# Optimization experiments

Hardware: AMD Instinct MI355X
Metric: run time of the kernel (lower is better)

The kernel has to match this reference:

```python
import jax, jax.numpy as jnp
import numpy as np

NEG_INF = -1e30  # stand-in for float('-inf'); avoids inf-inf NaN edge cases, same softmax result


def setup_inputs() -> dict:
    key = jax.random.key(0)
    k1, k2, k3, k4, k5 = jax.random.split(key, 5)
    B, T, C, H = 16, 2048, 200, 64
    x = jax.random.normal(k1, (B, T, C), dtype=jnp.float32)
    # padding mask over key positions, broadcastable to [B, T, T]
    padding_mask = jax.random.randint(k2, (B, 1, T), 0, 2, dtype=jnp.int32)
    # nn.Linear(n_embd, head_size, bias=False) weights, stored as [C, H] so y = x @ W
    Wk = jax.random.normal(k3, (C, H), dtype=jnp.float32) * (C ** -0.5)
    Wq = jax.random.normal(k4, (C, H), dtype=jnp.float32) * (C ** -0.5)
    Wv = jax.random.normal(k5, (C, H), dtype=jnp.float32) * (C ** -0.5)
    return {"x": x, "padding_mask": padding_mask, "Wk": Wk, "Wq": Wq, "Wv": Wv}


def reference(x, padding_mask, Wk, Wq, Wv):
    # x: [B,T,C]; padding_mask: [B,1,T] (0 = padded key position)
    k = x @ Wk  # [B,T,H]
    q = x @ Wq  # [B,T,H]
    v = x @ Wv  # [B,T,H]
    scale = k.shape[-1] ** -0.5
    wei = jnp.einsum("bqh,bkh->bqk", q, k) * scale  # [B,T,T]
    # mask padded key columns before softmax
    wei = jnp.where(padding_mask == 0, NEG_INF, wei)
    wei = jax.nn.softmax(wei, axis=-1)
    # mask padded query rows (transpose of padding mask) to exact zero after softmax
    mask_t = jnp.swapaxes(padding_mask, -2, -1)  # [B,T,1]
    wei = jnp.where(mask_t == 0, 0.0, wei)
    # dropout is identity in eval mode
    out = jnp.einsum("bqk,bkh->bqh", wei, v)  # [B,T,H]
    return out
```

## Files before the change

### kernel.cpp

```cpp
#include <hip/hip_runtime.h>


typedef __attribute__((ext_vector_type(8))) __bf16 bf16x8;
typedef __attribute__((ext_vector_type(4))) __bf16 bf16x4;
typedef __attribute__((ext_vector_type(4))) float f32x4;

#define T_SEQ 2048
#define C_DIM 200
#define H_DIM 64
#define BT_TOT 32768
#define QKV_ELEMS 2097152
#define PPAD 72
#define OPAD 68
#define WTF_FULL 36864
#define WTF_ELEMS 38400
#define WTF_A_ELEMS 24576
#define LOG2E 1.44269504088896f

__global__ void prep_w(const float* __restrict__ Wk, const float* __restrict__ Wq,
                       const float* __restrict__ Wv, __bf16* __restrict__ WtF) {
    int idx = blockIdx.x * 256 + threadIdx.x;
    if (idx >= WTF_ELEMS) return;
    int w, c, h;
    if (idx < WTF_FULL) {
        int j = idx & 7, lane = (idx >> 3) & 63;
        int chunk = idx >> 9;
        int t = chunk & 3, rest = chunk >> 2;
        w = rest % 3; int ks = rest / 3;
        c = ks * 32 + (lane >> 4) * 8 + j;
        h = t * 16 + (lane & 15);
    } else {
        int i2 = idx - WTF_FULL;
        int j = i2 & 7, l15 = (i2 >> 3) & 15, t = (i2 >> 7) & 3;
        w = i2 >> 9;
        c = 192 + j;
        h = t * 16 + l15;
    }
    const float* W = (w == 0) ? Wq : (w == 1) ? Wk : Wv;
    float val = W[c * H_DIM + h];
    if (w == 0) val *= 0.125f * LOG2E;
    WtF[idx] = (__bf16)val;
}

__global__ __launch_bounds__(256) void qkv_proj(const float* __restrict__ x,
                                                const __bf16* __restrict__ WtF,
                                                __bf16* __restrict__ qb,
                                                __bf16* __restrict__ kb,
                                                __bf16* __restrict__ vT) {
    __shared__ __bf16 Wl[WTF_A_ELEMS];

    const int tid = threadIdx.x;
    const int wave = tid >> 6, lane = tid & 63, l15 = lane & 15, quad = lane >> 4;
    const int m0b = blockIdx.x * 64;
    const int row0 = m0b + wave * 16;

    f32x4 acc[3][4] = {};

    #pragma unroll
    for (int i = 0; i < 12; ++i) {
        const int c = i * 256 + tid;
        *(bf16x8*)(Wl + c * 8) = *(const bf16x8*)(WtF + c * 8);
    }
    __syncthreads();
    #pragma unroll
    for (int ks = 0; ks < 4; ++ks) {
        const float* xr = x + (size_t)(row0 + l15) * C_DIM + ks * 32 + quad * 8;
        const float4 f0 = *(const float4*)xr;
        const float4 f1 = *(const float4*)(xr + 4);
        bf16x8 a;
        a[0]=(__bf16)f0.x; a[1]=(__bf16)f0.y; a[2]=(__bf16)f0.z; a[3]=(__bf16)f0.w;
        a[4]=(__bf16)f1.x; a[5]=(__bf16)f1.y; a[6]=(__bf16)f1.z; a[7]=(__bf16)f1.w;
        #pragma unroll
        for (int w = 0; w < 3; ++w)
            #pragma unroll
            for (int t = 0; t < 4; ++t) {
                const bf16x8 bf = *(const bf16x8*)(Wl + ((ks * 12 + w * 4 + t) << 9) + lane * 8);
                acc[w][t] = __builtin_amdgcn_mfma_f32_16x16x32_bf16(a, bf, acc[w][t], 0, 0, 0);
            }
    }
    __syncthreads();

    #pragma unroll
    for (int i = 0; i < 7; ++i) {
        const int c = i * 256 + tid;
        if (c < 1728)
            *(bf16x8*)(Wl + c * 8) = *(const bf16x8*)(WtF + WTF_A_ELEMS + c * 8);
    }
    __syncthreads();
    #pragma unroll
    for (int ks = 4; ks < 7; ++ks) {
        bf16x8 a;
        if (ks < 6 || quad == 0) {
            const float* xr = x + (size_t)(row0 + l15) * C_DIM + ks * 32 + quad * 8;
            const float4 f0 = *(const float4*)xr;
            const float4 f1 = *(const float4*)(xr + 4);
            a[0]=(__bf16)f0.x; a[1]=(__bf16)f0.y; a[2]=(__bf16)f0.z; a[3]=(__bf16)f0.w;
            a[4]=(__bf16)f1.x; a[5]=(__bf16)f1.y; a[6]=(__bf16)f1.z; a[7]=(__bf16)f1.w;
        } else {
            #pragma unroll
            for (int j = 0; j < 8; ++j) a[j] = (__bf16)0.f;
        }
        #pragma unroll
        for (int w = 0; w < 3; ++w)
            #pragma unroll
            for (int t = 0; t < 4; ++t) {
                const int off = (ks < 6) ? (((ks - 4) * 12 + w * 4 + t) << 9) + lane * 8
                                         : 12288 + ((w * 4 + t) << 7) + l15 * 8;
                const bf16x8 bf = *(const bf16x8*)(Wl + off);
                acc[w][t] = __builtin_amdgcn_mfma_f32_16x16x32_bf16(a, bf, acc[w][t], 0, 0, 0);
            }
    }

    #pragma unroll
    for (int t = 0; t < 4; ++t)
        #pragma unroll
        for (int r = 0; r < 4; ++r) {
            const size_t m = row0 + quad * 4 + r;
            qb[m * H_DIM + t * 16 + l15] = (__bf16)acc[0][t][r];
            kb[m * H_DIM + t * 16 + l15] = (__bf16)acc[1][t][r];
        }
    __syncthreads();
    #pragma unroll
    for (int t = 0; t < 4; ++t)
        #pragma unroll
        for (int r = 0; r < 4; ++r)
            Wl[(t * 16 + l15) * 72 + wave * 16 + quad * 4 + r] = (__bf16)acc[2][t][r];
    __syncthreads();
    const int bb = m0b >> 11, tloc = m0b & 2047;
    #pragma unroll
    for (int i = 0; i < 2; ++i) {
        const int seg = i * 256 + tid;
        const int h = seg >> 3, s8 = seg & 7;
        *(bf16x8*)(vT + ((size_t)bb * H_DIM + h) * T_SEQ + tloc + s8 * 8) =
            *(const bf16x8*)(Wl + h * 72 + s8 * 8);
    }
}

__global__ __launch_bounds__(256, 2) void attn(const __bf16* __restrict__ qb,
                                               const __bf16* __restrict__ kb,
                                               const __bf16* __restrict__ vT,
                                               const int* __restrict__ pm,
                                               float* __restrict__ out) {
    __shared__ __align__(16) char arena[8192 + 36864];
    float* biasS = (float*)arena;

    const int tid = threadIdx.x;
    const int wave = tid >> 6, lane = tid & 63, l15 = lane & 15, quad = lane >> 4;
    const int ks = wave;
    const int b = blockIdx.y;
    const int q0 = blockIdx.x * 64;
    const size_t bT = (size_t)b * T_SEQ;

    for (int i = tid; i < 512; i += 256) {
        const int4 p4 = *(const int4*)(pm + bT + i * 4);
        biasS[i * 4 + 0] = p4.x ? 0.f : -1e30f;
        biasS[i * 4 + 1] = p4.y ? 0.f : -1e30f;
        biasS[i * 4 + 2] = p4.z ? 0.f : -1e30f;
        biasS[i * 4 + 3] = p4.w ? 0.f : -1e30f;
    }
    __syncthreads();

    bf16x8 qa[4][2];
    #pragma unroll
    for (int mt = 0; mt < 4; ++mt)
        #pragma unroll
        for (int s = 0; s < 2; ++s)
            qa[mt][s] = *(const bf16x8*)(qb + (bT + q0 + mt * 16 + l15) * H_DIM + s * 32 + quad * 8);

    __bf16* P = (__bf16*)(arena + 8192) + wave * (64 * PPAD);
    const __bf16* kbase = kb + bT * H_DIM;
    const __bf16* vbase = vT + (size_t)b * H_DIM * T_SEQ;

    f32x4 oacc[4][4] = {};
    float lsum[4] = {0.f, 0.f, 0.f, 0.f};

    bf16x8 kf[8];
    #pragma unroll
    for (int n = 0; n < 4; ++n)
        #pragma unroll
        for (int s = 0; s < 2; ++s)
            kf[n * 2 + s] = *(const bf16x8*)(kbase + (ks * 512 + n * 16 + l15) * H_DIM + s * 32 + quad * 8);

    for (int kt = 0; kt < 8; ++kt) {
        const int key0 = ks * 512 + kt * 64;

        bf16x8 vf[8];
        #pragma unroll
        for (int t = 0; t < 4; ++t)
            #pragma unroll
            for (int s = 0; s < 2; ++s)
                vf[t * 2 + s] = *(const bf16x8*)(vbase + (size_t)(t * 16 + l15) * T_SEQ + key0 + s * 32 + quad * 8);

        #pragma unroll
        for (int n = 0; n < 4; ++n) {
            const f32x4 bias = *(const f32x4*)(biasS + key0 + n * 16 + quad * 4);
            f32x4 s_[4];
            #pragma unroll
            for (int mt = 0; mt < 4; ++mt) s_[mt] = bias;
            #pragma unroll
            for (int s = 0; s < 2; ++s)
                #pragma unroll
                for (int mt = 0; mt < 4; ++mt)
                    s_[mt] = __builtin_amdgcn_mfma_f32_16x16x32_bf16(kf[n * 2 + s], qa[mt][s], s_[mt], 0, 0, 0);
            #pragma unroll
            for (int mt = 0; mt < 4; ++mt) {
                bf16x4 p4;
                #pragma unroll
                for (int r = 0; r < 4; ++r) {
                    const float e = exp2f(s_[mt][r]);
                    lsum[mt] += e;
                    p4[r] = (__bf16)e;
                }
                *(bf16x4*)(P + (mt * 16 + l15) * PPAD + n * 16 + quad * 4) = p4;
            }
        }

        const int keyn = ks * 512 + ((kt < 7) ? kt + 1 : 7) * 64;
        #pragma unroll
        for (int n = 0; n < 4; ++n)
            #pragma unroll
            for (int s = 0; s < 2; ++s)
                kf[n * 2 + s] = *(const bf16x8*)(kbase + (keyn + n * 16 + l15) * H_DIM + s * 32 + quad * 8);

        bf16x8 pa[4][2];
        #pragma unroll
        for (int mt = 0; mt < 4; ++mt)
            #pragma unroll
            for (int s = 0; s < 2; ++s)
                pa[mt][s] = *(const bf16x8*)(P + (mt * 16 + l15) * PPAD + s * 32 + quad * 8);

        #pragma unroll
        for (int t = 0; t < 4; ++t)
            #pragma unroll
            for (int s = 0; s < 2; ++s)
                #pragma unroll
                for (int mt = 0; mt < 4; ++mt)
                    oacc[mt][t] = __builtin_amdgcn_mfma_f32_16x16x32_bf16(pa[mt][s], vf[t * 2 + s], oacc[mt][t], 0, 0, 0);
    }

    #pragma unroll
    for (int mt = 0; mt < 4; ++mt) {
        lsum[mt] += __shfl_xor(lsum[mt], 16, 64);
        lsum[mt] += __shfl_xor(lsum[mt], 32, 64);
    }

    float* Ocomb = (float*)(arena + 8192);
    float* Lcomb = Ocomb + 64 * OPAD;

    __syncthreads();
    if (ks == 1) {
        #pragma unroll
        for (int mt = 0; mt < 4; ++mt) {
            #pragma unroll
            for (int t = 0; t < 4; ++t)
                #pragma unroll
                for (int r = 0; r < 4; ++r)
                    Ocomb[(mt * 16 + quad * 4 + r) * OPAD + t * 16 + l15] = oacc[mt][t][r];
            if (quad == 0) Lcomb[mt * 16 + l15] = lsum[mt];
        }
    }
    __syncthreads();
    if (ks == 2) {
        #pragma unroll
        for (int mt = 0; mt < 4; ++mt) {
            #pragma unroll
            for (int t = 0; t < 4; ++t)
                #pragma unroll
                for (int r = 0; r < 4; ++r)
                    Ocomb[(mt * 16 + quad * 4 + r) * OPAD + t * 16 + l15] += oacc[mt][t][r];
            if (quad == 0) Lcomb[mt * 16 + l15] += lsum[mt];
        }
    }
    __syncthreads();
    if (ks == 3) {
        #pragma unroll
        for (int mt = 0; mt < 4; ++mt) {
            #pragma unroll
            for (int t = 0; t < 4; ++t)
                #pragma unroll
                for (int r = 0; r < 4; ++r)
                    Ocomb[(mt * 16 + quad * 4 + r) * OPAD + t * 16 + l15] += oacc[mt][t][r];
            if (quad == 0) Lcomb[mt * 16 + l15] += lsum[mt];
        }
    }
    __syncthreads();
    if (ks == 0) {
        #pragma unroll
        for (int mt = 0; mt < 4; ++mt) {
            lsum[mt] += Lcomb[mt * 16 + l15];
            #pragma unroll
            for (int t = 0; t < 4; ++t)
                #pragma unroll
                for (int r = 0; r < 4; ++r)
                    oacc[mt][t][r] += Ocomb[(mt * 16 + quad * 4 + r) * OPAD + t * 16 + l15];
            #pragma unroll
            for (int r = 0; r < 4; ++r) {
                const int qpos = q0 + mt * 16 + quad * 4 + r;
                const float lv = __shfl(lsum[mt], quad * 4 + r, 64);
                const bool qvalid = biasS[qpos] == 0.f;
                const float inv = (qvalid && lv > 0.f) ? 1.f / lv : 0.f;
                #pragma unroll
                for (int t = 0; t < 4; ++t)
                    out[(bT + qpos) * H_DIM + t * 16 + l15] = oacc[mt][t][r] * inv;
            }
        }
    }
}

extern "C" void kernel_launch(void* const* d_in, const int* in_sizes, int n_in,
                              void* d_out, int out_size, void* d_ws, size_t ws_size,
                              hipStream_t stream) {
    const float* x  = (const float*)d_in[0];
    const int* pm   = (const int*)d_in[1];
    const float* Wk = (const float*)d_in[2];
    const float* Wq = (const float*)d_in[3];
    const float* Wv = (const float*)d_in[4];
    float* out = (float*)d_out;

    __bf16* qb  = (__bf16*)d_ws;
    __bf16* kb  = qb + QKV_ELEMS;
    __bf16* vT  = kb + QKV_ELEMS;
    __bf16* WtF = vT + QKV_ELEMS;

    prep_w<<<dim3((WTF_ELEMS + 255) / 256), dim3(256), 0, stream>>>(Wk, Wq, Wv, WtF);
    qkv_proj<<<dim3(BT_TOT / 64), dim3(256), 0, stream>>>(x, WtF, qb, kb, vT);
    attn<<<dim3(T_SEQ / 64, 16), dim3(256), 0, stream>>>(qb, kb, vT, pm, out);
}
```

Baseline: 124.5 us.

## Enlarge QKV projection blocks, stage outputs in LDS, compute row sums via MFMA

```diff
diff --git a/kernel.cpp b/kernel.cpp
--- a/kernel.cpp
+++ b/kernel.cpp
@@ -42,23 +42,24 @@
     WtF[idx] = (__bf16)val;
 }
 
-__global__ __launch_bounds__(256) void qkv_proj(const float* __restrict__ x,
-                                                const __bf16* __restrict__ WtF,
-                                                __bf16* __restrict__ qb,
-                                                __bf16* __restrict__ kb,
-                                                __bf16* __restrict__ vT) {
-    __shared__ __bf16 Wl[WTF_A_ELEMS];
+__global__ __launch_bounds__(512, 2) void qkv_proj(const float* __restrict__ x,
+                                                   const __bf16* __restrict__ WtF,
+                                                   __bf16* __restrict__ qb,
+                                                   __bf16* __restrict__ kb,
+                                                   __bf16* __restrict__ vT) {
+    __shared__ __align__(16) char qarena[55296];
+    __bf16* Wl = (__bf16*)qarena;
 
     const int tid = threadIdx.x;
     const int wave = tid >> 6, lane = tid & 63, l15 = lane & 15, quad = lane >> 4;
-    const int m0b = blockIdx.x * 64;
+    const int m0b = blockIdx.x * 128;
     const int row0 = m0b + wave * 16;
 
     f32x4 acc[3][4] = {};
 
     #pragma unroll
-    for (int i = 0; i < 12; ++i) {
-        const int c = i * 256 + tid;
+    for (int i = 0; i < 6; ++i) {
+        const int c = i * 512 + tid;
         *(bf16x8*)(Wl + c * 8) = *(const bf16x8*)(WtF + c * 8);
     }
     __syncthreads();
@@ -81,8 +82,8 @@
     __syncthreads();
 
     #pragma unroll
-    for (int i = 0; i < 7; ++i) {
-        const int c = i * 256 + tid;
+    for (int i = 0; i < 4; ++i) {
+        const int c = i * 512 + tid;
         if (c < 1728)
             *(bf16x8*)(Wl + c * 8) = *(const bf16x8*)(WtF + WTF_A_ELEMS + c * 8);
     }
@@ -111,32 +112,47 @@
             }
     }
 
-    #pragma unroll
-    for (int t = 0; t < 4; ++t)
-        #pragma unroll
-        for (int r = 0; r < 4; ++r) {
-            const size_t m = row0 + quad * 4 + r;
-            qb[m * H_DIM + t * 16 + l15] = (__bf16)acc[0][t][r];
-            kb[m * H_DIM + t * 16 + l15] = (__bf16)acc[1][t][r];
-        }
-    __syncthreads();
-    #pragma unroll
-    for (int t = 0; t < 4; ++t)
-        #pragma unroll
-        for (int r = 0; r < 4; ++r)
-            Wl[(t * 16 + l15) * 72 + wave * 16 + quad * 4 + r] = (__bf16)acc[2][t][r];
-    __syncthreads();
-    const int bb = m0b >> 11, tloc = m0b & 2047;
-    #pragma unroll
-    for (int i = 0; i < 2; ++i) {
-        const int seg = i * 256 + tid;
-        const int h = seg >> 3, s8 = seg & 7;
-        *(bf16x8*)(vT + ((size_t)bb * H_DIM + h) * T_SEQ + tloc + s8 * 8) =
-            *(const bf16x8*)(Wl + h * 72 + s8 * 8);
+    __syncthreads();
+    {
+        __bf16* Lq = (__bf16*)qarena;
+        __bf16* Lk = Lq + 9216;
+        __bf16* Lv = Lk + 9216;
+        #pragma unroll
+        for (int t = 0; t < 4; ++t)
+            #pragma unroll
+            for (int r = 0; r < 4; ++r) {
+                const int mloc = wave * 16 + quad * 4 + r;
+                Lq[mloc * 72 + t * 16 + l15] = (__bf16)acc[0][t][r];
+                Lk[mloc * 72 + t * 16 + l15] = (__bf16)acc[1][t][r];
+                Lv[(t * 16 + l15) * 136 + mloc] = (__bf16)acc[2][t][r];
+            }
+    }
+    __syncthreads();
+    {
+        const __bf16* Lq = (const __bf16*)qarena;
+        const __bf16* Lk = Lq + 9216;
+        const __bf16* Lv = Lk + 9216;
+        const int bb = m0b >> 11, tloc = m0b & 2047;
+        #pragma unroll
+        for (int i = 0; i < 2; ++i) {
+            const int seg = i * 512 + tid;
+            const int row = seg >> 3, s8 = seg & 7;
+            *(bf16x8*)(qb + (size_t)(m0b + row) * H_DIM + s8 * 8) =
+                *(const bf16x8*)(Lq + row * 72 + s8 * 8);
+            *(bf16x8*)(kb + (size_t)(m0b + row) * H_DIM + s8 * 8) =
+                *(const bf16x8*)(Lk + row * 72 + s8 * 8);
+        }
+        #pragma unroll
+        for (int i = 0; i < 2; ++i) {
+            const int seg = i * 512 + tid;
+            const int h = seg >> 4, s16 = seg & 15;
+            *(bf16x8*)(vT + ((size_t)bb * H_DIM + h) * T_SEQ + tloc + s16 * 8) =
+                *(const bf16x8*)(Lv + h * 136 + s16 * 8);
+        }
     }
 }
 
-__global__ __launch_bounds__(256, 2) void attn(const __bf16* __restrict__ qb,
+__global__ __launch_bounds__(256, 3) void attn(const __bf16* __restrict__ qb,
                                                const __bf16* __restrict__ kb,
                                                const __bf16* __restrict__ vT,
                                                const int* __restrict__ pm,
@@ -167,33 +183,27 @@
         for (int s = 0; s < 2; ++s)
             qa[mt][s] = *(const bf16x8*)(qb + (bT + q0 + mt * 16 + l15) * H_DIM + s * 32 + quad * 8);
 
+    bf16x8 ones;
+    #pragma unroll
+    for (int j = 0; j < 8; ++j) ones[j] = (__bf16)1.0f;
+
     __bf16* P = (__bf16*)(arena + 8192) + wave * (64 * PPAD);
     const __bf16* kbase = kb + bT * H_DIM;
     const __bf16* vbase = vT + (size_t)b * H_DIM * T_SEQ;
 
     f32x4 oacc[4][4] = {};
-    float lsum[4] = {0.f, 0.f, 0.f, 0.f};
-
-    bf16x8 kf[8];
-    #pragma unroll
-    for (int n = 0; n < 4; ++n)
-        #pragma unroll
-        for (int s = 0; s < 2; ++s)
-            kf[n * 2 + s] = *(const bf16x8*)(kbase + (ks * 512 + n * 16 + l15) * H_DIM + s * 32 + quad * 8);
+    f32x4 oaccL[4] = {};
 
     for (int kt = 0; kt < 8; ++kt) {
         const int key0 = ks * 512 + kt * 64;
 
-        bf16x8 vf[8];
-        #pragma unroll
-        for (int t = 0; t < 4; ++t)
-            #pragma unroll
-            for (int s = 0; s < 2; ++s)
-                vf[t * 2 + s] = *(const bf16x8*)(vbase + (size_t)(t * 16 + l15) * T_SEQ + key0 + s * 32 + quad * 8);
-
         #pragma unroll
         for (int n = 0; n < 4; ++n) {
             const f32x4 bias = *(const f32x4*)(biasS + key0 + n * 16 + quad * 4);
+            bf16x8 kf[2];
+            #pragma unroll
+            for (int s = 0; s < 2; ++s)
+                kf[s] = *(const bf16x8*)(kbase + (key0 + n * 16 + l15) * H_DIM + s * 32 + quad * 8);
             f32x4 s_[4];
             #pragma unroll
             for (int mt = 0; mt < 4; ++mt) s_[mt] = bias;
@@ -201,27 +211,17 @@
             for (int s = 0; s < 2; ++s)
                 #pragma unroll
                 for (int mt = 0; mt < 4; ++mt)
-                    s_[mt] = __builtin_amdgcn_mfma_f32_16x16x32_bf16(kf[n * 2 + s], qa[mt][s], s_[mt], 0, 0, 0);
+                    s_[mt] = __builtin_amdgcn_mfma_f32_16x16x32_bf16(kf[s], qa[mt][s], s_[mt], 0, 0, 0);
             #pragma unroll
             for (int mt = 0; mt < 4; ++mt) {
                 bf16x4 p4;
                 #pragma unroll
-                for (int r = 0; r < 4; ++r) {
-                    const float e = exp2f(s_[mt][r]);
-                    lsum[mt] += e;
-                    p4[r] = (__bf16)e;
-                }
+                for (int r = 0; r < 4; ++r)
+                    p4[r] = (__bf16)exp2f(s_[mt][r]);
                 *(bf16x4*)(P + (mt * 16 + l15) * PPAD + n * 16 + quad * 4) = p4;
             }
         }
 
-        const int keyn = ks * 512 + ((kt < 7) ? kt + 1 : 7) * 64;
-        #pragma unroll
-        for (int n = 0; n < 4; ++n)
-            #pragma unroll
-            for (int s = 0; s < 2; ++s)
-                kf[n * 2 + s] = *(const bf16x8*)(kbase + (keyn + n * 16 + l15) * H_DIM + s * 32 + quad * 8);
-
         bf16x8 pa[4][2];
         #pragma unroll
         for (int mt = 0; mt < 4; ++mt)
@@ -230,22 +230,27 @@
                 pa[mt][s] = *(const bf16x8*)(P + (mt * 16 + l15) * PPAD + s * 32 + quad * 8);
 
         #pragma unroll
-        for (int t = 0; t < 4; ++t)
+        for (int s = 0; s < 2; ++s)
+            #pragma unroll
+            for (int mt = 0; mt < 4; ++mt)
+                oaccL[mt] = __builtin_amdgcn_mfma_f32_16x16x32_bf16(pa[mt][s], ones, oaccL[mt], 0, 0, 0);
+
+        #pragma unroll
+        for (int t = 0; t < 4; ++t) {
+            bf16x8 vf[2];
+            #pragma unroll
+            for (int s = 0; s < 2; ++s)
+                vf[s] = *(const bf16x8*)(vbase + (size_t)(t * 16 + l15) * T_SEQ + key0 + s * 32 + quad * 8);
             #pragma unroll
             for (int s = 0; s < 2; ++s)
                 #pragma unroll
                 for (int mt = 0; mt < 4; ++mt)
-                    oacc[mt][t] = __builtin_amdgcn_mfma_f32_16x16x32_bf16(pa[mt][s], vf[t * 2 + s], oacc[mt][t], 0, 0, 0);
-    }
-
-    #pragma unroll
-    for (int mt = 0; mt < 4; ++mt) {
-        lsum[mt] += __shfl_xor(lsum[mt], 16, 64);
-        lsum[mt] += __shfl_xor(lsum[mt], 32, 64);
+                    oacc[mt][t] = __builtin_amdgcn_mfma_f32_16x16x32_bf16(pa[mt][s], vf[s], oacc[mt][t], 0, 0, 0);
+        }
     }
 
     float* Ocomb = (float*)(arena + 8192);
-    float* Lcomb = Ocomb + 64 * OPAD;
+    float* Lcomb = (float*)(arena + 8192 + 17408);
 
     __syncthreads();
     if (ks == 1) {
@@ -256,7 +261,11 @@
                 #pragma unroll
                 for (int r = 0; r < 4; ++r)
                     Ocomb[(mt * 16 + quad * 4 + r) * OPAD + t * 16 + l15] = oacc[mt][t][r];
-            if (quad == 0) Lcomb[mt * 16 + l15] = lsum[mt];
+            if (l15 == 0) {
+                #pragma unroll
+                for (int r = 0; r < 4; ++r)
+                    Lcomb[mt * 16 + quad * 4 + r] = oaccL[mt][r];
+            }
         }
     }
     __syncthreads();
@@ -268,7 +277,11 @@
                 #pragma unroll
                 for (int r = 0; r < 4; ++r)
                     Ocomb[(mt * 16 + quad * 4 + r) * OPAD + t * 16 + l15] += oacc[mt][t][r];
-            if (quad == 0) Lcomb[mt * 16 + l15] += lsum[mt];
+            if (l15 == 0) {
+                #pragma unroll
+                for (int r = 0; r < 4; ++r)
+                    Lcomb[mt * 16 + quad * 4 + r] += oaccL[mt][r];
+            }
         }
     }
     __syncthreads();
@@ -280,28 +293,28 @@
                 #pragma unroll
                 for (int r = 0; r < 4; ++r)
                     Ocomb[(mt * 16 + quad * 4 + r) * OPAD + t * 16 + l15] += oacc[mt][t][r];
-            if (quad == 0) Lcomb[mt * 16 + l15] += lsum[mt];
+            if (l15 == 0) {
+                #pragma unroll
+                for (int r = 0; r < 4; ++r)
+                    Lcomb[mt * 16 + quad * 4 + r] += oaccL[mt][r];
+            }
         }
     }
     __syncthreads();
     if (ks == 0) {
         #pragma unroll
         for (int mt = 0; mt < 4; ++mt) {
-            lsum[mt] += Lcomb[mt * 16 + l15];
-            #pragma unroll
-            for (int t = 0; t < 4; ++t)
-                #pragma unroll
-                for (int r = 0; r < 4; ++r)
-                    oacc[mt][t][r] += Ocomb[(mt * 16 + quad * 4 + r) * OPAD + t * 16 + l15];
             #pragma unroll
             for (int r = 0; r < 4; ++r) {
-                const int qpos = q0 + mt * 16 + quad * 4 + r;
-                const float lv = __shfl(lsum[mt], quad * 4 + r, 64);
+                const int rw = mt * 16 + quad * 4 + r;
+                const int qpos = q0 + rw;
+                const float lv = oaccL[mt][r] + Lcomb[rw];
                 const bool qvalid = biasS[qpos] == 0.f;
                 const float inv = (qvalid && lv > 0.f) ? 1.f / lv : 0.f;
                 #pragma unroll
                 for (int t = 0; t < 4; ++t)
-                    out[(bT + qpos) * H_DIM + t * 16 + l15] = oacc[mt][t][r] * inv;
+                    out[(bT + qpos) * H_DIM + t * 16 + l15] =
+                        (oacc[mt][t][r] + Ocomb[rw * OPAD + t * 16 + l15]) * inv;
             }
         }
     }
@@ -323,6 +336,6 @@
     __bf16* WtF = vT + QKV_ELEMS;
 
     prep_w<<<dim3((WTF_ELEMS + 255) / 256), dim3(256), 0, stream>>>(Wk, Wq, Wv, WtF);
-    qkv_proj<<<dim3(BT_TOT / 64), dim3(256), 0, stream>>>(x, WtF, qb, kb, vT);
+    qkv_proj<<<dim3(BT_TOT / 128), dim3(512), 0, stream>>>(x, WtF, qb, kb, vT);
     attn<<<dim3(T_SEQ / 64, 16), dim3(256), 0, stream>>>(qb, kb, vT, pm, out);
 }
```

New measurement: 131.6 us. 1.06x slower.
